# Kernel optimization log

Hardware: AMD Instinct MI355X
Metric: run time of the kernel (lower is better)

Reference implementation:

```python
import jax, jax.numpy as jnp
import numpy as np

B, C, H, W = 2, 1024, 64, 64
R, E, HE, T, K = 16, 4, 512, 3, 2


def setup_inputs() -> dict:
    key = jax.random.key(0)
    ks = jax.random.split(key, 12)
    s = 0.02
    return {
        "x": jax.random.normal(ks[0], (B, C, H, W), jnp.float32),
        "t": jax.random.normal(ks[1], (B, C, H, W), jnp.float32),
        "fc_w": jax.random.normal(ks[2], (C, 2 * C), jnp.float32) * s,
        "ln_g": jnp.ones((C,), jnp.float32),
        "ln_b": jnp.zeros((C,), jnp.float32),
        "f1_w1": jax.random.normal(ks[3], (C // R, C), jnp.float32) * s,
        "f1_b1": jnp.zeros((C // R,), jnp.float32),
        "f1_wa": jax.random.normal(ks[4], (C, C // R), jnp.float32) * s,
        "f1_ba": jnp.zeros((C,), jnp.float32),
        "f1_wb": jax.random.normal(ks[5], (C, C // R), jnp.float32) * s,
        "f1_bb": jnp.zeros((C,), jnp.float32),
        "w_gate": jax.random.normal(ks[6], (T, C, E), jnp.float32) * s,
        "e_w1": jax.random.normal(ks[7], (E, C, HE), jnp.float32) * s,
        "e_b1": jnp.zeros((E, HE), jnp.float32),
        "e_w2": jax.random.normal(ks[8], (E, HE, C), jnp.float32) * s,
        "e_b2": jnp.zeros((E, C), jnp.float32),
        "task_index": 1,
    }


def _cv_squared(v):
    eps = 1e-10
    return jnp.var(v, ddof=1) / (jnp.mean(v) ** 2 + eps)


def reference(x, t, fc_w, ln_g, ln_b, f1_w1, f1_b1, f1_wa, f1_ba, f1_wb, f1_bb,
              w_gate, e_w1, e_b1, e_w2, e_b2, task_index):
    b, c, h, w = x.shape
    n = h * w
    # MultiTaskGeneralFusion: SE-style dual-branch channel gating
    s = jnp.mean(x + t, axis=(2, 3))                        # [B, C]
    hid = jax.nn.relu(s @ f1_w1.T + f1_b1)                  # [B, C/r]
    a = hid @ f1_wa.T + f1_ba                               # [B, C]
    bb = hid @ f1_wb.T + f1_bb                              # [B, C]
    wts = jax.nn.softmax(jnp.stack([a, bb], axis=0), axis=0)  # [2, B, C]
    z = wts[0][:, :, None, None] * x + wts[1][:, :, None, None] * t
    # fused linear -> ReLU -> LayerNorm on concatenated tokens
    x3 = x.reshape(b, c, n).transpose(0, 2, 1)              # [B, N, C]
    t3 = t.reshape(b, c, n).transpose(0, 2, 1)
    y = jnp.concatenate([x3, t3], axis=-1)                  # [B, N, 2C]
    y = jax.nn.relu(jnp.einsum('bnd,cd->bnc', y, fc_w))     # [B, N, C]
    mu = jnp.mean(y, axis=-1, keepdims=True)
    var = jnp.mean((y - mu) ** 2, axis=-1, keepdims=True)
    y = (y - mu) * jax.lax.rsqrt(var + 1e-5) * ln_g + ln_b
    yf = y.reshape(b * n, c)                                # [BN, C]
    # MMoE top-k gating (eval mode: no gating noise)
    logits = yf @ w_gate[task_index]                        # [BN, E]
    top_logits, top_idx = jax.lax.top_k(logits, K)          # [BN, K]
    top_gates = jax.nn.softmax(top_logits, axis=-1)
    gates = jnp.zeros_like(logits).at[jnp.arange(b * n)[:, None], top_idx].set(top_gates)
    # dense expert compute, gated combine
    eh = jax.nn.relu(jnp.einsum('nc,ech->neh', yf, e_w1) + e_b1)   # [BN, E, HE]
    eo = jnp.einsum('neh,eho->neo', eh, e_w2) + e_b2               # [BN, E, C]
    ym = jnp.einsum('ne,neo->no', gates, eo)                        # [BN, C]
    importance = gates.sum(axis=0)
    load = (gates > 0).sum(axis=0).astype(jnp.float32)
    aux_loss = _cv_squared(importance) + _cv_squared(load)
    y4 = ym.reshape(b, n, c).transpose(0, 2, 1).reshape(b, c, h, w) + z
    return (y4, aux_loss)
```

## Files before the change

### kernel.cpp

```cpp
#include <hip/hip_runtime.h>
#include <cstddef>
#include <cstdint>

#define B_   2
#define C_   1024
#define N_   4096
#define M_   8192
#define K2_  2048
#define E_   4
#define HE_  512

typedef float f32x4 __attribute__((ext_vector_type(4)));
typedef short bf16x8 __attribute__((ext_vector_type(8)));
typedef _Float16 f16x8 __attribute__((ext_vector_type(8)));
typedef unsigned short u16x8 __attribute__((ext_vector_type(8)));

static __device__ __forceinline__ unsigned short f2bf(float f) {
  unsigned int u = __float_as_uint(f);
  u = u + 0x7fffu + ((u >> 16) & 1u);
  return (unsigned short)(u >> 16);
}

static __device__ __forceinline__ void gl_lds16(const void* g, void* l) {
  __builtin_amdgcn_global_load_lds(
      (const __attribute__((address_space(1))) void*)(uintptr_t)g,
      (__attribute__((address_space(3))) void*)(unsigned)(uintptr_t)l,
      16, 0, 0);
}

__global__ __launch_bounds__(256) void k_reduce_s(const float* __restrict__ x,
                                                  const float* __restrict__ t,
                                                  float* __restrict__ s) {
  const int bc = blockIdx.x;
  const float* xp = x + (size_t)bc * N_;
  const float* tp = t + (size_t)bc * N_;
  float acc = 0.f;
  for (int i = threadIdx.x; i < N_ / 4; i += 256) {
    const float4 a = ((const float4*)xp)[i];
    const float4 b = ((const float4*)tp)[i];
    acc += ((a.x + b.x) + (a.y + b.y)) + ((a.z + b.z) + (a.w + b.w));
  }
  #pragma unroll
  for (int o = 32; o; o >>= 1) acc += __shfl_down(acc, o);
  __shared__ float red[4];
  if ((threadIdx.x & 63) == 0) red[threadIdx.x >> 6] = acc;
  __syncthreads();
  if (threadIdx.x == 0)
    s[bc] = (red[0] + red[1] + red[2] + red[3]) * (1.f / (float)N_);
}

__global__ __launch_bounds__(256) void k_se_gate(const float* __restrict__ s,
                                                 const float* __restrict__ w1, const float* __restrict__ b1,
                                                 const float* __restrict__ wa, const float* __restrict__ ba,
                                                 const float* __restrict__ wb, const float* __restrict__ bbv,
                                                 float* __restrict__ wts0) {
  __shared__ float hid[2][64];
  const int t = threadIdx.x;
  if (t < 128) {
    const int b = t >> 6, r = t & 63;
    float acc = b1[r];
    const float* sp = s + b * C_;
    const float* wp = w1 + r * C_;
    for (int c = 0; c < C_; ++c) acc = fmaf(sp[c], wp[c], acc);
    hid[b][r] = fmaxf(acc, 0.f);
  }
  __syncthreads();
  for (int o = t; o < B_ * C_; o += 256) {
    const int b = o >> 10, c = o & 1023;
    float a = ba[c], bb = bbv[c];
    #pragma unroll 8
    for (int r = 0; r < 64; ++r) {
      const float h = hid[b][r];
      a  = fmaf(h, wa[c * 64 + r], a);
      bb = fmaf(h, wb[c * 64 + r], bb);
    }
    wts0[o] = 1.f / (1.f + expf(bb - a));
  }
}

__global__ __launch_bounds__(256) void k_prep_act(const float* __restrict__ x,
                                                  const float* __restrict__ t,
                                                  _Float16* __restrict__ ah,
                                                  _Float16* __restrict__ am) {
  __shared__ float tile[64][65];
  const int c0 = blockIdx.x * 64, n0 = blockIdx.y * 64, b = blockIdx.z;
  const float* xb = x + (size_t)b * (C_ * N_);
  const float* tb = t + (size_t)b * (C_ * N_);
  _Float16* ahb = ah + (size_t)b * (N_ * (size_t)K2_);
  _Float16* amb = am + (size_t)b * (N_ * (size_t)K2_);
  const int tid = threadIdx.x;
  #pragma unroll
  for (int srcsel = 0; srcsel < 2; ++srcsel) {
    const float* src = srcsel ? tb : xb;
    const int koff = srcsel ? C_ : 0;
    if (srcsel) __syncthreads();
    #pragma unroll
    for (int p = 0; p < 4; ++p) {
      const int f = tid + p * 256;
      const int cr = f >> 4, nq = f & 15;
      const float4 v = *(const float4*)(src + (size_t)(c0 + cr) * N_ + n0 + nq * 4);
      tile[cr][nq * 4 + 0] = v.x; tile[cr][nq * 4 + 1] = v.y;
      tile[cr][nq * 4 + 2] = v.z; tile[cr][nq * 4 + 3] = v.w;
    }
    __syncthreads();
    #pragma unroll
    for (int p = 0; p < 2; ++p) {
      const int f = tid + p * 256;
      const int mr = f >> 3, kq = f & 7;
      f16x8 hv, mv;
      #pragma unroll
      for (int u = 0; u < 8; ++u) {
        const float v = tile[kq * 8 + u][mr] * 64.f;
        const _Float16 h = (_Float16)v;
        hv[u] = h;
        mv[u] = (_Float16)(v - (float)h);
      }
      const size_t off = (size_t)(n0 + mr) * K2_ + koff + c0 + kq * 8;
      *(f16x8*)(ahb + off) = hv;
      *(f16x8*)(amb + off) = mv;
    }
  }
}

__global__ __launch_bounds__(256) void k_prep_fcw(const float* __restrict__ w,
                                                  _Float16* __restrict__ wh,
                                                  _Float16* __restrict__ wm) {
  const size_t i = ((size_t)blockIdx.x * 256 + threadIdx.x) * 8;
  const float4 v0 = *(const float4*)(w + i);
  const float4 v1 = *(const float4*)(w + i + 4);
  const float vv[8] = {v0.x, v0.y, v0.z, v0.w, v1.x, v1.y, v1.z, v1.w};
  f16x8 hv, mv;
  #pragma unroll
  for (int u = 0; u < 8; ++u) {
    const float sv = vv[u] * 4096.f;
    const _Float16 h = (_Float16)sv;
    hv[u] = h;
    mv[u] = (_Float16)(sv - (float)h);
  }
  *(f16x8*)(wh + i) = hv;
  *(f16x8*)(wm + i) = mv;
}

__global__ __launch_bounds__(256) void k_prep_tr(const float* __restrict__ src, long long zs, int srs,
                                                 unsigned short* __restrict__ dst, long long zo, int drs) {
  __shared__ float tile[64][65];
  const int c0 = blockIdx.x * 64, r0 = blockIdx.y * 64, z = blockIdx.z;
  const float* s = src + (size_t)z * zs;
  unsigned short* d = dst + (size_t)z * zo;
  const int tid = threadIdx.x;
  #pragma unroll
  for (int p = 0; p < 4; ++p) {
    const int f = tid + p * 256;
    const int rr = f >> 4, cq = f & 15;
    const float4 v = *(const float4*)(s + (size_t)(r0 + rr) * srs + c0 + cq * 4);
    tile[rr][cq * 4 + 0] = v.x; tile[rr][cq * 4 + 1] = v.y;
    tile[rr][cq * 4 + 2] = v.z; tile[rr][cq * 4 + 3] = v.w;
  }
  __syncthreads();
  #pragma unroll
  for (int p = 0; p < 2; ++p) {
    const int f = tid + p * 256;
    const int cr = f >> 3, rq = f & 7;
    u16x8 o;
    #pragma unroll
    for (int u = 0; u < 8; ++u) o[u] = f2bf(tile[rq * 8 + u][cr]);
    *(u16x8*)(d + (size_t)(c0 + cr) * drs + r0 + rq * 8) = o;
  }
}

__global__ __launch_bounds__(256) void k_fc_mfma(const _Float16* __restrict__ Ah,
                                                 const _Float16* __restrict__ Am,
                                                 const _Float16* __restrict__ Bh,
                                                 const _Float16* __restrict__ Bm,
                                                 float* __restrict__ y) {
  __shared__ __align__(16) _Float16 lA[2][2][4096];
  __shared__ __align__(16) _Float16 lB[2][2][4096];
  const int tid = threadIdx.x, w = tid >> 6, l = tid & 63;
  const int m0 = blockIdx.y * 128, n0 = blockIdx.x * 128;
  const int wr = w >> 1, wc = w & 1, lg = l >> 4, lr = l & 15;
  f32x4 acc[4][4] = {};

  auto STAGE = [&](int buf, int k0) {
    #pragma unroll
    for (int p = 0; p < 2; ++p) {
      const int c = w * 2 + p;
      const int i = c * 64 + l;
      const int g = i >> 7, row = i & 127;
      const size_t ga = (size_t)(m0 + row) * K2_ + k0 + g * 8;
      const size_t gb = (size_t)(n0 + row) * K2_ + k0 + g * 8;
      char* dA = (char*)lA + buf * 16384 + c * 1024;
      char* dB = (char*)lB + buf * 16384 + c * 1024;
      gl_lds16(Ah + ga, dA);
      gl_lds16(Am + ga, dA + 8192);
      gl_lds16(Bh + gb, dB);
      gl_lds16(Bm + gb, dB + 8192);
    }
  };

  STAGE(0, 0);
  __syncthreads();
  for (int k0 = 0; k0 < K2_; k0 += 32) {
    const int cur = (k0 >> 5) & 1;
    if (k0 + 32 < K2_) STAGE(cur ^ 1, k0 + 32);
    f16x8 ah[4], am[4], bh[4], bm[4];
    #pragma unroll
    for (int i = 0; i < 4; ++i) {
      const int off = (lg * 128 + wr * 64 + i * 16 + lr) * 8;
      ah[i] = *(const f16x8*)((char*)lA + cur * 16384 + off * 2);
      am[i] = *(const f16x8*)((char*)lA + cur * 16384 + 8192 + off * 2);
    }
    #pragma unroll
    for (int j = 0; j < 4; ++j) {
      const int off = (lg * 128 + wc * 64 + j * 16 + lr) * 8;
      bh[j] = *(const f16x8*)((char*)lB + cur * 16384 + off * 2);
      bm[j] = *(const f16x8*)((char*)lB + cur * 16384 + 8192 + off * 2);
    }
    #pragma unroll
    for (int i = 0; i < 4; ++i)
      #pragma unroll
      for (int j = 0; j < 4; ++j)
        acc[i][j] = __builtin_amdgcn_mfma_f32_16x16x32_f16(ah[i], bh[j], acc[i][j], 0, 0, 0);
    #pragma unroll
    for (int i = 0; i < 4; ++i)
      #pragma unroll
      for (int j = 0; j < 4; ++j)
        acc[i][j] = __builtin_amdgcn_mfma_f32_16x16x32_f16(ah[i], bm[j], acc[i][j], 0, 0, 0);
    #pragma unroll
    for (int i = 0; i < 4; ++i)
      #pragma unroll
      for (int j = 0; j < 4; ++j)
        acc[i][j] = __builtin_amdgcn_mfma_f32_16x16x32_f16(am[i], bh[j], acc[i][j], 0, 0, 0);
    __syncthreads();
  }
  #pragma unroll
  for (int i = 0; i < 4; ++i) {
    const int mb = m0 + wr * 64 + i * 16 + lg * 4;
    #pragma unroll
    for (int j = 0; j < 4; ++j) {
      const int n = n0 + wc * 64 + j * 16 + lr;
      #pragma unroll
      for (int r = 0; r < 4; ++r)
        y[(size_t)(mb + r) * C_ + n] = fmaxf(acc[i][j][r] * (1.f / 262144.f), 0.f);
    }
  }
}

__global__ __launch_bounds__(256) void k_ln_topk(const float* __restrict__ y,
                                                 const float* __restrict__ lng, const float* __restrict__ lnb,
                                                 const float* __restrict__ wg, const int* __restrict__ taskp,
                                                 unsigned short* __restrict__ yf, float* __restrict__ gates) {
  const int wv = threadIdx.x >> 6, ln = threadIdx.x & 63;
  const int m = blockIdx.x * 4 + wv;
  const float* yr = y + (size_t)m * C_;
  float4 v[4];
  #pragma unroll
  for (int ch = 0; ch < 4; ++ch) v[ch] = *(const float4*)(yr + ch * 256 + ln * 4);
  float sum = 0.f;
  #pragma unroll
  for (int ch = 0; ch < 4; ++ch) sum += (v[ch].x + v[ch].y) + (v[ch].z + v[ch].w);
  #pragma unroll
  for (int o = 32; o; o >>= 1) sum += __shfl_down(sum, o);
  sum = __shfl(sum, 0);
  const float mu = sum * (1.f / 1024.f);
  float q = 0.f;
  #pragma unroll
  for (int ch = 0; ch < 4; ++ch) {
    const float dx = v[ch].x - mu, dy = v[ch].y - mu, dz = v[ch].z - mu, dw = v[ch].w - mu;
    q += (dx * dx + dy * dy) + (dz * dz + dw * dw);
  }
  #pragma unroll
  for (int o = 32; o; o >>= 1) q += __shfl_down(q, o);
  q = __shfl(q, 0);
  const float rstd = rsqrtf(q * (1.f / 1024.f) + 1e-5f);
  const float* wrow = wg + (size_t)(*taskp) * (C_ * E_);
  float l0 = 0.f, l1 = 0.f, l2 = 0.f, l3 = 0.f;
  #pragma unroll
  for (int ch = 0; ch < 4; ++ch) {
    const int c = ch * 256 + ln * 4;
    const float4 gg = *(const float4*)(lng + c);
    const float4 bv = *(const float4*)(lnb + c);
    float f[4];
    f[0] = (v[ch].x - mu) * rstd * gg.x + bv.x;
    f[1] = (v[ch].y - mu) * rstd * gg.y + bv.y;
    f[2] = (v[ch].z - mu) * rstd * gg.z + bv.z;
    f[3] = (v[ch].w - mu) * rstd * gg.w + bv.w;
    uint2 pk;
    pk.x = (unsigned)f2bf(f[0]) | ((unsigned)f2bf(f[1]) << 16);
    pk.y = (unsigned)f2bf(f[2]) | ((unsigned)f2bf(f[3]) << 16);
    *(uint2*)(yf + (size_t)m * C_ + c) = pk;
    #pragma unroll
    for (int i = 0; i < 4; ++i) {
      const float4 we = *(const float4*)(wrow + (size_t)(c + i) * 4);
      l0 = fmaf(f[i], we.x, l0); l1 = fmaf(f[i], we.y, l1);
      l2 = fmaf(f[i], we.z, l2); l3 = fmaf(f[i], we.w, l3);
    }
  }
  #pragma unroll
  for (int o = 32; o; o >>= 1) {
    l0 += __shfl_down(l0, o); l1 += __shfl_down(l1, o);
    l2 += __shfl_down(l2, o); l3 += __shfl_down(l3, o);
  }
  if (ln == 0) {
    const float L[4] = {l0, l1, l2, l3};
    int i1 = 0; float best = L[0];
    #pragma unroll
    for (int e = 1; e < 4; ++e) if (L[e] > best) { best = L[e]; i1 = e; }
    int i2 = -1; float s2 = 0.f;
    #pragma unroll
    for (int e = 0; e < 4; ++e) if (e != i1 && (i2 < 0 || L[e] > s2)) { s2 = L[e]; i2 = e; }
    const float g1 = 1.f / (1.f + expf(s2 - best));
    const float g2 = 1.f - g1;
    float4 gv;
    gv.x = (i1 == 0) ? g1 : ((i2 == 0) ? g2 : 0.f);
    gv.y = (i1 == 1) ? g1 : ((i2 == 1) ? g2 : 0.f);
    gv.z = (i1 == 2) ? g1 : ((i2 == 2) ? g2 : 0.f);
    gv.w = (i1 == 3) ? g1 : ((i2 == 3) ? g2 : 0.f);
    *(float4*)(gates + (size_t)m * 4) = gv;
  }
}

__global__ __launch_bounds__(256) void k_moe1_mfma(const unsigned short* __restrict__ yf,
                                                   const short* __restrict__ Bw,
                                                   const float* __restrict__ b1,
                                                   const float* __restrict__ gates,
                                                   unsigned short* __restrict__ ehg) {
  __shared__ __align__(16) short lA[2][4096], lB[2][4096];
  const int tid = threadIdx.x, w = tid >> 6, l = tid & 63;
  const int m0 = blockIdx.y * 128, n0 = blockIdx.x * 128;
  const int wr = w >> 1, wc = w & 1, lg = l >> 4, lr = l & 15;
  f32x4 acc[4][4] = {};

  auto STAGE = [&](int buf, int k0) {
    #pragma unroll
    for (int p = 0; p < 2; ++p) {
      const int c = w * 2 + p;
      const int i = c * 64 + l;
      const int g = i >> 7, row = i & 127;
      gl_lds16(yf + (size_t)(m0 + row) * C_ + k0 + g * 8, (char*)lA + buf * 8192 + c * 1024);
      gl_lds16(Bw + (size_t)(n0 + row) * C_ + k0 + g * 8, (char*)lB + buf * 8192 + c * 1024);
    }
  };

  STAGE(0, 0);
  __syncthreads();
  for (int k0 = 0; k0 < C_; k0 += 32) {
    const int cur = (k0 >> 5) & 1;
    if (k0 + 32 < C_) STAGE(cur ^ 1, k0 + 32);
    bf16x8 af[4], bfr[4];
    #pragma unroll
    for (int i = 0; i < 4; ++i)
      af[i] = *(const bf16x8*)((char*)lA + cur * 8192 + (lg * 128 + wr * 64 + i * 16 + lr) * 16);
    #pragma unroll
    for (int j = 0; j < 4; ++j)
      bfr[j] = *(const bf16x8*)((char*)lB + cur * 8192 + (lg * 128 + wc * 64 + j * 16 + lr) * 16);
    #pragma unroll
    for (int i = 0; i < 4; ++i)
      #pragma unroll
      for (int j = 0; j < 4; ++j)
        acc[i][j] = __builtin_amdgcn_mfma_f32_16x16x32_bf16(af[i], bfr[j], acc[i][j], 0, 0, 0);
    __syncthreads();
  }
  const int e0 = n0 >> 9;
  #pragma unroll
  for (int j = 0; j < 4; ++j) {
    const int n = n0 + wc * 64 + j * 16 + lr;
    const float bias = b1[e0 * HE_ + (n & 511)];
    #pragma unroll
    for (int i = 0; i < 4; ++i) {
      const int mb = m0 + wr * 64 + i * 16 + lg * 4;
      #pragma unroll
      for (int r = 0; r < 4; ++r) {
        const float g = gates[(size_t)(mb + r) * 4 + e0];
        const float v = fmaxf(acc[i][j][r] + bias, 0.f) * g;
        ehg[(size_t)(mb + r) * K2_ + n] = f2bf(v);
      }
    }
  }
}

__global__ __launch_bounds__(256) void k_moe2_mfma(const short* __restrict__ Aeh,
                                                   const short* __restrict__ Bw,
                                                   const float* __restrict__ b2,
                                                   const float* __restrict__ gates,
                                                   float* __restrict__ ym) {
  __shared__ __align__(16) short lA[2][4096], lB[2][4096];
  const int tid = threadIdx.x, w = tid >> 6, l = tid & 63;
  const int m0 = blockIdx.y * 128, n0 = blockIdx.x * 128;
  const int wr = w >> 1, wc = w & 1, lg = l >> 4, lr = l & 15;
  f32x4 acc[4][4] = {};

  auto STAGE = [&](int buf, int k0) {
    #pragma unroll
    for (int p = 0; p < 2; ++p) {
      const int c = w * 2 + p;
      const int i = c * 64 + l;
      const int g = i >> 7, row = i & 127;
      gl_lds16(Aeh + (size_t)(m0 + row) * K2_ + k0 + g * 8, (char*)lA + buf * 8192 + c * 1024);
      gl_lds16(Bw + (size_t)(n0 + row) * K2_ + k0 + g * 8, (char*)lB + buf * 8192 + c * 1024);
    }
  };

  STAGE(0, 0);
  __syncthreads();
  for (int k0 = 0; k0 < K2_; k0 += 32) {
    const int cur = (k0 >> 5) & 1;
    if (k0 + 32 < K2_) STAGE(cur ^ 1, k0 + 32);
    bf16x8 af[4], bfr[4];
    #pragma unroll
    for (int i = 0; i < 4; ++i)
      af[i] = *(const bf16x8*)((char*)lA + cur * 8192 + (lg * 128 + wr * 64 + i * 16 + lr) * 16);
    #pragma unroll
    for (int j = 0; j < 4; ++j)
      bfr[j] = *(const bf16x8*)((char*)lB + cur * 8192 + (lg * 128 + wc * 64 + j * 16 + lr) * 16);
    #pragma unroll
    for (int i = 0; i < 4; ++i)
      #pragma unroll
      for (int j = 0; j < 4; ++j)
        acc[i][j] = __builtin_amdgcn_mfma_f32_16x16x32_bf16(af[i], bfr[j], acc[i][j], 0, 0, 0);
    __syncthreads();
  }
  float bb[4][4];
  #pragma unroll
  for (int j = 0; j < 4; ++j) {
    const int n = n0 + wc * 64 + j * 16 + lr;
    #pragma unroll
    for (int e = 0; e < 4; ++e) bb[j][e] = b2[e * C_ + n];
  }
  #pragma unroll
  for (int i = 0; i < 4; ++i) {
    const int mb = m0 + wr * 64 + i * 16 + lg * 4;
    #pragma unroll
    for (int r = 0; r < 4; ++r) {
      const float4 g = *(const float4*)(gates + (size_t)(mb + r) * 4);
      #pragma unroll
      for (int j = 0; j < 4; ++j) {
        const int n = n0 + wc * 64 + j * 16 + lr;
        ym[(size_t)(mb + r) * C_ + n] =
            acc[i][j][r] + g.x * bb[j][0] + g.y * bb[j][1] + g.z * bb[j][2] + g.w * bb[j][3];
      }
    }
  }
}

__global__ __launch_bounds__(256) void k_aux(const float* __restrict__ gates, float* __restrict__ outp) {
  const int t = threadIdx.x;
  float imp[4] = {0, 0, 0, 0}, ld[4] = {0, 0, 0, 0};
  for (int m = t; m < M_; m += 256) {
    const float4 g = *(const float4*)(gates + (size_t)m * 4);
    imp[0] += g.x; imp[1] += g.y; imp[2] += g.z; imp[3] += g.w;
    ld[0] += (g.x > 0.f) ? 1.f : 0.f; ld[1] += (g.y > 0.f) ? 1.f : 0.f;
    ld[2] += (g.z > 0.f) ? 1.f : 0.f; ld[3] += (g.w > 0.f) ? 1.f : 0.f;
  }
  __shared__ float red[8][4];
  const int wv = t >> 6, ln = t & 63;
  #pragma unroll
  for (int e = 0; e < 4; ++e) {
    float a = imp[e], b = ld[e];
    #pragma unroll
    for (int o = 32; o; o >>= 1) { a += __shfl_down(a, o); b += __shfl_down(b, o); }
    if (ln == 0) { red[e][wv] = a; red[4 + e][wv] = b; }
  }
  __syncthreads();
  if (t == 0) {
    float I[4], L[4];
    #pragma unroll
    for (int e = 0; e < 4; ++e) {
      I[e] = red[e][0] + red[e][1] + red[e][2] + red[e][3];
      L[e] = red[4 + e][0] + red[4 + e][1] + red[4 + e][2] + red[4 + e][3];
    }
    const float mi = (I[0] + I[1] + I[2] + I[3]) * 0.25f;
    const float vi = ((I[0] - mi) * (I[0] - mi) + (I[1] - mi) * (I[1] - mi) +
                      (I[2] - mi) * (I[2] - mi) + (I[3] - mi) * (I[3] - mi)) / 3.f;
    const float ml = (L[0] + L[1] + L[2] + L[3]) * 0.25f;
    const float vl = ((L[0] - ml) * (L[0] - ml) + (L[1] - ml) * (L[1] - ml) +
                      (L[2] - ml) * (L[2] - ml) + (L[3] - ml) * (L[3] - ml)) / 3.f;
    *outp = vi / (mi * mi + 1e-10f) + vl / (ml * ml + 1e-10f);
  }
}

__global__ __launch_bounds__(256) void k_final(const float* __restrict__ ym,
                                               const float* __restrict__ x, const float* __restrict__ t,
                                               const float* __restrict__ wts0, float* __restrict__ out) {
  __shared__ float tile[64][65];
  const int c0 = blockIdx.x * 64, n0 = blockIdx.y * 64, b = blockIdx.z;
  const int tid = threadIdx.x;
  #pragma unroll
  for (int p = 0; p < 4; ++p) {
    const int f = tid + p * 256;
    const int row = f >> 4, cq = f & 15;
    const float4 v = *(const float4*)(ym + (size_t)(b * N_ + n0 + row) * C_ + c0 + cq * 4);
    tile[row][cq * 4 + 0] = v.x; tile[row][cq * 4 + 1] = v.y;
    tile[row][cq * 4 + 2] = v.z; tile[row][cq * 4 + 3] = v.w;
  }
  __syncthreads();
  #pragma unroll
  for (int p = 0; p < 4; ++p) {
    const int f = tid + p * 256;
    const int cr = f >> 4, nq = f & 15;
    const int c = c0 + cr;
    const float w0 = wts0[b * C_ + c];
    const float w1 = 1.f - w0;
    const size_t idx = (size_t)(b * C_ + c) * N_ + n0 + nq * 4;
    const float4 xv = *(const float4*)(x + idx);
    const float4 tv = *(const float4*)(t + idx);
    float4 o;
    o.x = tile[nq * 4 + 0][cr] + w0 * xv.x + w1 * tv.x;
    o.y = tile[nq * 4 + 1][cr] + w0 * xv.y + w1 * tv.y;
    o.z = tile[nq * 4 + 2][cr] + w0 * xv.z + w1 * tv.z;
    o.w = tile[nq * 4 + 3][cr] + w0 * xv.w + w1 * tv.w;
    *(float4*)(out + idx) = o;
  }
}

extern "C" void kernel_launch(void* const* d_in, const int* in_sizes, int n_in,
                              void* d_out, int out_size, void* d_ws, size_t ws_size,
                              hipStream_t stream) {
  const float* x     = (const float*)d_in[0];
  const float* t     = (const float*)d_in[1];
  const float* fc_w  = (const float*)d_in[2];
  const float* ln_g  = (const float*)d_in[3];
  const float* ln_b  = (const float*)d_in[4];
  const float* f1_w1 = (const float*)d_in[5];
  const float* f1_b1 = (const float*)d_in[6];
  const float* f1_wa = (const float*)d_in[7];
  const float* f1_ba = (const float*)d_in[8];
  const float* f1_wb = (const float*)d_in[9];
  const float* f1_bb = (const float*)d_in[10];
  const float* w_gate = (const float*)d_in[11];
  const float* e_w1  = (const float*)d_in[12];
  const float* e_b1  = (const float*)d_in[13];
  const float* e_w2  = (const float*)d_in[14];
  const float* e_b2  = (const float*)d_in[15];
  const int*   task  = (const int*)d_in[16];
  float* out = (float*)d_out;

  char* ws = (char*)d_ws;
  float*          y    = (float*)ws;
  _Float16*       ah   = (_Float16*)(ws + 33554432);
  _Float16*       am   = (_Float16*)(ws + 67108864);
  unsigned short* yf   = (unsigned short*)(ws + 33554432);
  unsigned short* ehg  = (unsigned short*)(ws + 50331648);
  _Float16* wh  = (_Float16*)(ws + 100663296);
  _Float16* wm  = (_Float16*)(ws + 104857600);
  short*    w1t = (short*)(ws + 109051904);
  short*    w2t = (short*)(ws + 113246208);
  float* sbuf  = (float*)(ws + 117440512);
  float* wts0  = (float*)(ws + 117448704);
  float* gates = (float*)(ws + 117456896);

  k_reduce_s<<<B_ * C_, 256, 0, stream>>>(x, t, sbuf);
  k_se_gate<<<1, 256, 0, stream>>>(sbuf, f1_w1, f1_b1, f1_wa, f1_ba, f1_wb, f1_bb, wts0);
  k_prep_fcw<<<1024, 256, 0, stream>>>(fc_w, wh, wm);
  k_prep_tr<<<dim3(8, 16, 4), 256, 0, stream>>>(e_w1, 524288LL, 512, (unsigned short*)w1t, 524288LL, 1024);
  k_prep_tr<<<dim3(16, 8, 4), 256, 0, stream>>>(e_w2, 524288LL, 1024, (unsigned short*)w2t, 512LL, 2048);
  k_prep_act<<<dim3(16, 64, 2), 256, 0, stream>>>(x, t, ah, am);
  k_fc_mfma<<<dim3(8, 64), 256, 0, stream>>>(ah, am, wh, wm, y);
  k_ln_topk<<<M_ / 4, 256, 0, stream>>>(y, ln_g, ln_b, w_gate, task, yf, gates);
  k_moe1_mfma<<<dim3(16, 64), 256, 0, stream>>>(yf, w1t, e_b1, gates, ehg);
  k_moe2_mfma<<<dim3(8, 64), 256, 0, stream>>>((const short*)ehg, w2t, e_b2, gates, y);
  k_aux<<<1, 256, 0, stream>>>(gates, out + (size_t)B_ * C_ * N_);
  k_final<<<dim3(C_ / 64, N_ / 64, B_), 256, 0, stream>>>(y, x, t, wts0, out);
}
```

Before: 451.4 us.

## Prefetch two stages ahead with explicit vmcnt waits and swizzle tile order

The three MFMA GEMM kernels (fc, moe1, moe2) now issue global-to-LDS loads two k-steps ahead. They replace __syncthreads with explicit s_waitcnt vmcnt/lgkmcnt plus raw s_barrier, so loads for the next tile stay in flight while the current one is computed. The staging address math is simplified by precomputing per-thread base offsets. The block index is also remapped so consecutive workgroups share A/B tiles in cache. The hand-written wait counts are fragile if the number of loads per stage changes.

```diff
diff --git a/kernel.cpp b/kernel.cpp
--- a/kernel.cpp
+++ b/kernel.cpp
@@ -14,6 +14,9 @@
 typedef short bf16x8 __attribute__((ext_vector_type(8)));
 typedef _Float16 f16x8 __attribute__((ext_vector_type(8)));
 typedef unsigned short u16x8 __attribute__((ext_vector_type(8)));
+
+#define WAITV(N) asm volatile("s_waitcnt vmcnt(" #N ")" ::: "memory")
+#define WAITL0   asm volatile("s_waitcnt lgkmcnt(0)" ::: "memory")
 
 static __device__ __forceinline__ unsigned short f2bf(float f) {
   unsigned int u = __float_as_uint(f);
@@ -173,64 +176,69 @@
                                                  const _Float16* __restrict__ Bh,
                                                  const _Float16* __restrict__ Bm,
                                                  float* __restrict__ y) {
-  __shared__ __align__(16) _Float16 lA[2][2][4096];
-  __shared__ __align__(16) _Float16 lB[2][2][4096];
+  __shared__ __align__(16) char lds[2][32768];
   const int tid = threadIdx.x, w = tid >> 6, l = tid & 63;
-  const int m0 = blockIdx.y * 128, n0 = blockIdx.x * 128;
+  const int flat = blockIdx.x + blockIdx.y * 8;
+  const int swz = (flat & 7) * 64 + (flat >> 3);
+  const int n0 = (swz & 7) * 128, m0 = (swz >> 3) * 128;
   const int wr = w >> 1, wc = w & 1, lg = l >> 4, lr = l & 15;
   f32x4 acc[4][4] = {};
+  const int sg = tid >> 7, sr = tid & 127;
+  const size_t ga0 = (size_t)(m0 + sr) * K2_ + sg * 8;
+  const size_t gb0 = (size_t)(n0 + sr) * K2_ + sg * 8;
 
   auto STAGE = [&](int buf, int k0) {
-    #pragma unroll
-    for (int p = 0; p < 2; ++p) {
-      const int c = w * 2 + p;
-      const int i = c * 64 + l;
-      const int g = i >> 7, row = i & 127;
-      const size_t ga = (size_t)(m0 + row) * K2_ + k0 + g * 8;
-      const size_t gb = (size_t)(n0 + row) * K2_ + k0 + g * 8;
-      char* dA = (char*)lA + buf * 16384 + c * 1024;
-      char* dB = (char*)lB + buf * 16384 + c * 1024;
-      gl_lds16(Ah + ga, dA);
-      gl_lds16(Am + ga, dA + 8192);
-      gl_lds16(Bh + gb, dB);
-      gl_lds16(Bm + gb, dB + 8192);
-    }
+    char* b = &lds[buf][0] + w * 1024;
+    gl_lds16(Ah + ga0 + k0, b);
+    gl_lds16(Ah + ga0 + 16 + k0, b + 4096);
+    gl_lds16(Am + ga0 + k0, b + 8192);
+    gl_lds16(Am + ga0 + 16 + k0, b + 12288);
+    gl_lds16(Bh + gb0 + k0, b + 16384);
+    gl_lds16(Bh + gb0 + 16 + k0, b + 20480);
+    gl_lds16(Bm + gb0 + k0, b + 24576);
+    gl_lds16(Bm + gb0 + 16 + k0, b + 28672);
   };
 
   STAGE(0, 0);
-  __syncthreads();
-  for (int k0 = 0; k0 < K2_; k0 += 32) {
-    const int cur = (k0 >> 5) & 1;
-    if (k0 + 32 < K2_) STAGE(cur ^ 1, k0 + 32);
-    f16x8 ah[4], am[4], bh[4], bm[4];
+  STAGE(1, 32);
+  for (int it = 0; it < 64; ++it) {
+    const int cur = it & 1;
+    if (it < 63) { WAITV(8); } else { WAITV(0); }
+    __builtin_amdgcn_sched_barrier(0);
+    __builtin_amdgcn_s_barrier();
+    const char* bb = &lds[cur][0];
+    f16x8 a_h[4], a_m[4], b_h[4], b_m[4];
     #pragma unroll
     for (int i = 0; i < 4; ++i) {
-      const int off = (lg * 128 + wr * 64 + i * 16 + lr) * 8;
-      ah[i] = *(const f16x8*)((char*)lA + cur * 16384 + off * 2);
-      am[i] = *(const f16x8*)((char*)lA + cur * 16384 + 8192 + off * 2);
+      const int off = lg * 2048 + (wr * 64 + i * 16 + lr) * 16;
+      a_h[i] = *(const f16x8*)(bb + off);
+      a_m[i] = *(const f16x8*)(bb + 8192 + off);
     }
     #pragma unroll
     for (int j = 0; j < 4; ++j) {
-      const int off = (lg * 128 + wc * 64 + j * 16 + lr) * 8;
-      bh[j] = *(const f16x8*)((char*)lB + cur * 16384 + off * 2);
-      bm[j] = *(const f16x8*)((char*)lB + cur * 16384 + 8192 + off * 2);
+      const int off = lg * 2048 + (wc * 64 + j * 16 + lr) * 16;
+      b_h[j] = *(const f16x8*)(bb + 16384 + off);
+      b_m[j] = *(const f16x8*)(bb + 24576 + off);
     }
     #pragma unroll
     for (int i = 0; i < 4; ++i)
       #pragma unroll
       for (int j = 0; j < 4; ++j)
-        acc[i][j] = __builtin_amdgcn_mfma_f32_16x16x32_f16(ah[i], bh[j], acc[i][j], 0, 0, 0);
+        acc[i][j] = __builtin_amdgcn_mfma_f32_16x16x32_f16(a_h[i], b_h[j], acc[i][j], 0, 0, 0);
     #pragma unroll
     for (int i = 0; i < 4; ++i)
       #pragma unroll
       for (int j = 0; j < 4; ++j)
-        acc[i][j] = __builtin_amdgcn_mfma_f32_16x16x32_f16(ah[i], bm[j], acc[i][j], 0, 0, 0);
+        acc[i][j] = __builtin_amdgcn_mfma_f32_16x16x32_f16(a_h[i], b_m[j], acc[i][j], 0, 0, 0);
     #pragma unroll
     for (int i = 0; i < 4; ++i)
       #pragma unroll
       for (int j = 0; j < 4; ++j)
-        acc[i][j] = __builtin_amdgcn_mfma_f32_16x16x32_f16(am[i], bh[j], acc[i][j], 0, 0, 0);
-    __syncthreads();
+        acc[i][j] = __builtin_amdgcn_mfma_f32_16x16x32_f16(a_m[i], b_h[j], acc[i][j], 0, 0, 0);
+    WAITL0;
+    __builtin_amdgcn_sched_barrier(0);
+    __builtin_amdgcn_s_barrier();
+    if (it < 62) STAGE(cur, (it + 2) * 32);
   }
   #pragma unroll
   for (int i = 0; i < 4; ++i) {
@@ -324,41 +332,49 @@
                                                    const float* __restrict__ b1,
                                                    const float* __restrict__ gates,
                                                    unsigned short* __restrict__ ehg) {
-  __shared__ __align__(16) short lA[2][4096], lB[2][4096];
+  __shared__ __align__(16) char lds[2][16384];
   const int tid = threadIdx.x, w = tid >> 6, l = tid & 63;
-  const int m0 = blockIdx.y * 128, n0 = blockIdx.x * 128;
+  const int flat = blockIdx.x + blockIdx.y * 16;
+  const int swz = (flat & 7) * 128 + (flat >> 3);
+  const int n0 = (swz & 15) * 128, m0 = (swz >> 4) * 128;
   const int wr = w >> 1, wc = w & 1, lg = l >> 4, lr = l & 15;
   f32x4 acc[4][4] = {};
+  const int sg = tid >> 7, sr = tid & 127;
+  const size_t ga0 = (size_t)(m0 + sr) * C_ + sg * 8;
+  const size_t gb0 = (size_t)(n0 + sr) * C_ + sg * 8;
 
   auto STAGE = [&](int buf, int k0) {
-    #pragma unroll
-    for (int p = 0; p < 2; ++p) {
-      const int c = w * 2 + p;
-      const int i = c * 64 + l;
-      const int g = i >> 7, row = i & 127;
-      gl_lds16(yf + (size_t)(m0 + row) * C_ + k0 + g * 8, (char*)lA + buf * 8192 + c * 1024);
-      gl_lds16(Bw + (size_t)(n0 + row) * C_ + k0 + g * 8, (char*)lB + buf * 8192 + c * 1024);
-    }
+    char* b = &lds[buf][0] + w * 1024;
+    gl_lds16(yf + ga0 + k0, b);
+    gl_lds16(yf + ga0 + 16 + k0, b + 4096);
+    gl_lds16(Bw + gb0 + k0, b + 8192);
+    gl_lds16(Bw + gb0 + 16 + k0, b + 12288);
   };
 
   STAGE(0, 0);
-  __syncthreads();
-  for (int k0 = 0; k0 < C_; k0 += 32) {
-    const int cur = (k0 >> 5) & 1;
-    if (k0 + 32 < C_) STAGE(cur ^ 1, k0 + 32);
+  STAGE(1, 32);
+  for (int it = 0; it < 32; ++it) {
+    const int cur = it & 1;
+    if (it < 31) { WAITV(4); } else { WAITV(0); }
+    __builtin_amdgcn_sched_barrier(0);
+    __builtin_amdgcn_s_barrier();
+    const char* bb = &lds[cur][0];
     bf16x8 af[4], bfr[4];
     #pragma unroll
     for (int i = 0; i < 4; ++i)
-      af[i] = *(const bf16x8*)((char*)lA + cur * 8192 + (lg * 128 + wr * 64 + i * 16 + lr) * 16);
+      af[i] = *(const bf16x8*)(bb + lg * 2048 + (wr * 64 + i * 16 + lr) * 16);
     #pragma unroll
     for (int j = 0; j < 4; ++j)
-      bfr[j] = *(const bf16x8*)((char*)lB + cur * 8192 + (lg * 128 + wc * 64 + j * 16 + lr) * 16);
+      bfr[j] = *(const bf16x8*)(bb + 8192 + lg * 2048 + (wc * 64 + j * 16 + lr) * 16);
     #pragma unroll
     for (int i = 0; i < 4; ++i)
       #pragma unroll
       for (int j = 0; j < 4; ++j)
         acc[i][j] = __builtin_amdgcn_mfma_f32_16x16x32_bf16(af[i], bfr[j], acc[i][j], 0, 0, 0);
-    __syncthreads();
+    WAITL0;
+    __builtin_amdgcn_sched_barrier(0);
+    __builtin_amdgcn_s_barrier();
+    if (it < 30) STAGE(cur, (it + 2) * 32);
   }
   const int e0 = n0 >> 9;
   #pragma unroll
@@ -383,48 +399,56 @@
                                                    const float* __restrict__ b2,
                                                    const float* __restrict__ gates,
                                                    float* __restrict__ ym) {
-  __shared__ __align__(16) short lA[2][4096], lB[2][4096];
+  __shared__ __align__(16) char lds[2][16384];
   const int tid = threadIdx.x, w = tid >> 6, l = tid & 63;
-  const int m0 = blockIdx.y * 128, n0 = blockIdx.x * 128;
+  const int flat = blockIdx.x + blockIdx.y * 8;
+  const int swz = (flat & 7) * 64 + (flat >> 3);
+  const int n0 = (swz & 7) * 128, m0 = (swz >> 3) * 128;
   const int wr = w >> 1, wc = w & 1, lg = l >> 4, lr = l & 15;
   f32x4 acc[4][4] = {};
+  const int sg = tid >> 7, sr = tid & 127;
+  const size_t ga0 = (size_t)(m0 + sr) * K2_ + sg * 8;
+  const size_t gb0 = (size_t)(n0 + sr) * K2_ + sg * 8;
 
   auto STAGE = [&](int buf, int k0) {
-    #pragma unroll
-    for (int p = 0; p < 2; ++p) {
-      const int c = w * 2 + p;
-      const int i = c * 64 + l;
-      const int g = i >> 7, row = i & 127;
-      gl_lds16(Aeh + (size_t)(m0 + row) * K2_ + k0 + g * 8, (char*)lA + buf * 8192 + c * 1024);
-      gl_lds16(Bw + (size_t)(n0 + row) * K2_ + k0 + g * 8, (char*)lB + buf * 8192 + c * 1024);
-    }
+    char* b = &lds[buf][0] + w * 1024;
+    gl_lds16(Aeh + ga0 + k0, b);
+    gl_lds16(Aeh + ga0 + 16 + k0, b + 4096);
+    gl_lds16(Bw + gb0 + k0, b + 8192);
+    gl_lds16(Bw + gb0 + 16 + k0, b + 12288);
   };
 
   STAGE(0, 0);
-  __syncthreads();
-  for (int k0 = 0; k0 < K2_; k0 += 32) {
-    const int cur = (k0 >> 5) & 1;
-    if (k0 + 32 < K2_) STAGE(cur ^ 1, k0 + 32);
+  STAGE(1, 32);
+  for (int it = 0; it < 64; ++it) {
+    const int cur = it & 1;
+    if (it < 63) { WAITV(4); } else { WAITV(0); }
+    __builtin_amdgcn_sched_barrier(0);
+    __builtin_amdgcn_s_barrier();
+    const char* bb = &lds[cur][0];
     bf16x8 af[4], bfr[4];
     #pragma unroll
     for (int i = 0; i < 4; ++i)
-      af[i] = *(const bf16x8*)((char*)lA + cur * 8192 + (lg * 128 + wr * 64 + i * 16 + lr) * 16);
+      af[i] = *(const bf16x8*)(bb + lg * 2048 + (wr * 64 + i * 16 + lr) * 16);
     #pragma unroll
     for (int j = 0; j < 4; ++j)
-      bfr[j] = *(const bf16x8*)((char*)lB + cur * 8192 + (lg * 128 + wc * 64 + j * 16 + lr) * 16);
+      bfr[j] = *(const bf16x8*)(bb + 8192 + lg * 2048 + (wc * 64 + j * 16 + lr) * 16);
     #pragma unroll
     for (int i = 0; i < 4; ++i)
       #pragma unroll
       for (int j = 0; j < 4; ++j)
         acc[i][j] = __builtin_amdgcn_mfma_f32_16x16x32_bf16(af[i], bfr[j], acc[i][j], 0, 0, 0);
-    __syncthreads();
-  }
-  float bb[4][4];
+    WAITL0;
+    __builtin_amdgcn_sched_barrier(0);
+    __builtin_amdgcn_s_barrier();
+    if (it < 62) STAGE(cur, (it + 2) * 32);
+  }
+  float bb2[4][4];
   #pragma unroll
   for (int j = 0; j < 4; ++j) {
     const int n = n0 + wc * 64 + j * 16 + lr;
     #pragma unroll
-    for (int e = 0; e < 4; ++e) bb[j][e] = b2[e * C_ + n];
+    for (int e = 0; e < 4; ++e) bb2[j][e] = b2[e * C_ + n];
   }
   #pragma unroll
   for (int i = 0; i < 4; ++i) {
@@ -436,7 +460,7 @@
       for (int j = 0; j < 4; ++j) {
         const int n = n0 + wc * 64 + j * 16 + lr;
         ym[(size_t)(mb + r) * C_ + n] =
-            acc[i][j][r] + g.x * bb[j][0] + g.y * bb[j][1] + g.z * bb[j][2] + g.w * bb[j][3];
+            acc[i][j][r] + g.x * bb2[j][0] + g.y * bb2[j][1] + g.z * bb2[j][2] + g.w * bb2[j][3];
       }
     }
   }
```

Result: faster. 424.7 us (-5.9%).
